# Performance work log

Measured on AMD Instinct MI355X. Metric: run time of the kernel, lower is better.

## Reference

```python
import jax, jax.numpy as jnp
import numpy as np

G = 8
NEIGHBORS = 9
EPS = 1e-5


def grid_sample_bilinear_border(img, grid):
    # img: [B, C, H, W], grid: [B, Hg, Wg, 2] with (x, y) in [-1, 1]
    # matches torch.nn.functional.grid_sample(mode='bilinear', padding_mode='border', align_corners=False)
    B, C, H, W = img.shape
    gx, gy = grid[..., 0], grid[..., 1]
    ix = jnp.clip(((gx + 1.0) * W - 1.0) * 0.5, 0.0, W - 1.0)
    iy = jnp.clip(((gy + 1.0) * H - 1.0) * 0.5, 0.0, H - 1.0)
    x0 = jnp.floor(ix); y0 = jnp.floor(iy)
    x1 = x0 + 1.0;      y1 = y0 + 1.0
    w00 = (x1 - ix) * (y1 - iy)
    w01 = (ix - x0) * (y1 - iy)
    w10 = (x1 - ix) * (iy - y0)
    w11 = (ix - x0) * (iy - y0)
    x0i = jnp.clip(x0, 0, W - 1).astype(jnp.int32)
    x1i = jnp.clip(x1, 0, W - 1).astype(jnp.int32)
    y0i = jnp.clip(y0, 0, H - 1).astype(jnp.int32)
    y1i = jnp.clip(y1, 0, H - 1).astype(jnp.int32)

    def gather(im, yy, xx):  # im [C,H,W], yy/xx [Hg,Wg] -> [C,Hg,Wg]
        return im[:, yy, xx]

    g = jax.vmap(gather)
    out = (g(img, y0i, x0i) * w00[:, None]
         + g(img, y0i, x1i) * w01[:, None]
         + g(img, y1i, x0i) * w10[:, None]
         + g(img, y1i, x1i) * w11[:, None])
    return out  # [B, C, Hg, Wg]


def pconv(x, w):
    # 1x1x1 conv3d (no bias): x [B,Cin,D,H,W], w [Cout,Cin]
    return jnp.einsum('bcdhw,oc->bodhw', x, w)


def bn_relu(x, gamma, beta):
    # BatchNorm3d (training-mode batch stats, biased variance) + ReLU
    mean = jnp.mean(x, axis=(0, 2, 3, 4), keepdims=True)
    var = jnp.var(x, axis=(0, 2, 3, 4), keepdims=True)
    xn = (x - mean) * jax.lax.rsqrt(var + EPS)
    return jax.nn.relu(xn * gamma.reshape(1, -1, 1, 1, 1) + beta.reshape(1, -1, 1, 1, 1))


def setup_inputs() -> dict:
    key = jax.random.key(0)
    ks = jax.random.split(key, 8)
    B, C, H, W = 2, 64, 256, 320
    ref_feature = jax.random.normal(ks[0], (B, C, H, W), dtype=jnp.float32)
    grid = jax.random.uniform(ks[1], (B, NEIGHBORS * H, W, 2), dtype=jnp.float32,
                              minval=-1.0, maxval=1.0)
    s0 = 1.0 / np.sqrt(G)
    w0 = jax.random.uniform(ks[2], (16, G), jnp.float32, -s0, s0)
    g0 = jnp.ones((16,), jnp.float32); b0 = jnp.zeros((16,), jnp.float32)
    s1 = 1.0 / np.sqrt(16)
    w1 = jax.random.uniform(ks[3], (8, 16), jnp.float32, -s1, s1)
    g1 = jnp.ones((8,), jnp.float32); b1 = jnp.zeros((8,), jnp.float32)
    s2 = 1.0 / np.sqrt(8)
    ws = jax.random.uniform(ks[4], (1, 8), jnp.float32, -s2, s2)
    bs = jax.random.uniform(ks[5], (1,), jnp.float32, -s2, s2)
    return {"ref_feature": ref_feature, "grid": grid,
            "w0": w0, "g0": g0, "b0": b0,
            "w1": w1, "g1": g1, "b1": b1,
            "ws": ws, "bs": bs}


def reference(ref_feature, grid, w0, g0, b0, w1, g1, b1, ws, bs):
    B, C, H, W = ref_feature.shape
    x = grid_sample_bilinear_border(ref_feature, grid)          # [B, C, 9H, W]
    ref = ref_feature.reshape(B, G, C // G, H, W)               # [B, G, C/G, H, W]
    x = x.reshape(B, G, C // G, NEIGHBORS, H, W)
    x = jnp.mean(x * ref[:, :, :, None], axis=2)                # [B, G, 9, H, W]
    x = bn_relu(pconv(x, w0), g0, b0)                           # [B, 16, 9, H, W]
    x = bn_relu(pconv(x, w1), g1, b1)                           # [B, 8, 9, H, W]
    s = pconv(x, ws) + bs.reshape(1, -1, 1, 1, 1)               # [B, 1, 9, H, W]
    return jax.nn.sigmoid(jnp.squeeze(s, axis=1))               # [B, 9, H, W]
```

## Files before the change

kernel.cpp:

```cpp
#include <hip/hip_runtime.h>
#include <math.h>


constexpr int   Bc  = 2;
constexpr int   Cc  = 64;
constexpr int   Hc  = 256;
constexpr int   Wc  = 320;
constexpr int   NBc = 9;
constexpr int   HWc = Hc * Wc;
constexpr int   NPIX = Bc * HWc;
constexpr int   NPT  = Bc * NBc * HWc;
constexpr float EPSV = 1e-5f;

constexpr int NB1 = 512;
constexpr int NB2 = 512;

constexpr size_t OFF_FEATB = 0;
constexpr size_t OFF_S     = OFF_FEATB + (size_t)NPIX * 32;
constexpr size_t OFF_P1    = OFF_S + (size_t)NPT * 8;
constexpr size_t OFF_BN1   = OFF_P1 + (size_t)NB1 * 32;
constexpr size_t OFF_P2    = OFF_BN1 + 32;
constexpr size_t OFF_BN2   = OFF_P2 + (size_t)NB2 * 16;

__device__ __forceinline__ unsigned short f2bf_rne(float v) {
  unsigned int u = __float_as_uint(v);
  unsigned int r = (u + 0x7fffu + ((u >> 16) & 1u)) >> 16;
  return (unsigned short)r;
}

__global__ __launch_bounds__(256) void k_transpose(
    const float* __restrict__ feat, unsigned short* __restrict__ featB) {
  __shared__ float lds[64][65];
  const int tid  = threadIdx.x;
  const int b    = blockIdx.x / (HWc / 64);
  const int tile = blockIdx.x % (HWc / 64);
  const int hw0  = tile * 64;
  const int p    = tid & 63;
  const int ty   = tid >> 6;

  const float* src = feat + (size_t)b * Cc * HWc + hw0 + p;
#pragma unroll
  for (int c0 = 0; c0 < 64; c0 += 4) {
    lds[c0 + ty][p] = src[(size_t)(c0 + ty) * HWc];
  }
  __syncthreads();
  const int ch = tid & 63;
  unsigned short* dst = featB + ((size_t)b * HWc + hw0) * 64 + ch;
#pragma unroll
  for (int p0 = 0; p0 < 64; p0 += 4) {
    dst[(size_t)(p0 + ty) * 64] = f2bf_rne(lds[ch][p0 + ty]);
  }
}

__device__ __forceinline__ void unpack8(uint4 u, float f[8]) {
  f[0] = __uint_as_float(u.x << 16);
  f[1] = __uint_as_float(u.x & 0xffff0000u);
  f[2] = __uint_as_float(u.y << 16);
  f[3] = __uint_as_float(u.y & 0xffff0000u);
  f[4] = __uint_as_float(u.z << 16);
  f[5] = __uint_as_float(u.z & 0xffff0000u);
  f[6] = __uint_as_float(u.w << 16);
  f[7] = __uint_as_float(u.w & 0xffff0000u);
}

__global__ __launch_bounds__(256) void k_sample(
    const float* __restrict__ grid, const unsigned short* __restrict__ featB,
    const float* __restrict__ feat, float* __restrict__ sOut) {
  const int tid = threadIdx.x;
  const int cid = blockIdx.x * 32 + (tid >> 3);
  const int j   = tid & 7;
  const int b   = cid / HWc;
  const int hw  = cid - b * HWc;
  const int h   = hw / Wc;
  const int w   = hw - h * Wc;

  const float* rp = feat + ((size_t)b * Cc + j * 8) * HWc + hw;
  float r[8];
#pragma unroll
  for (int k = 0; k < 8; ++k) r[k] = rp[(size_t)k * HWc];

  const uint4* fb = (const uint4*)featB + (size_t)b * HWc * 8;

#pragma unroll 3
  for (int n = 0; n < NBc; ++n) {
    const size_t gi = ((((size_t)b * NBc + n) * Hc + h) * Wc + w) * 2;
    const float2 g2 = *(const float2*)(grid + gi);
    float ix = ((g2.x + 1.f) * (float)Wc - 1.f) * 0.5f;
    float iy = ((g2.y + 1.f) * (float)Hc - 1.f) * 0.5f;
    ix = fminf(fmaxf(ix, 0.f), (float)(Wc - 1));
    iy = fminf(fmaxf(iy, 0.f), (float)(Hc - 1));
    const float x0f = floorf(ix), y0f = floorf(iy);
    const float fx = ix - x0f, fy = iy - y0f;
    const int x0 = (int)x0f, y0 = (int)y0f;
    const int x1 = min(x0 + 1, Wc - 1), y1 = min(y0 + 1, Hc - 1);
    const float w00 = (1.f - fx) * (1.f - fy);
    const float w01 = fx * (1.f - fy);
    const float w10 = (1.f - fx) * fy;
    const float w11 = fx * fy;

    const uint4 u00 = fb[(size_t)(y0 * Wc + x0) * 8 + j];
    const uint4 u01 = fb[(size_t)(y0 * Wc + x1) * 8 + j];
    const uint4 u10 = fb[(size_t)(y1 * Wc + x0) * 8 + j];
    const uint4 u11 = fb[(size_t)(y1 * Wc + x1) * 8 + j];
    float a[8], c[8], d[8], e[8];
    unpack8(u00, a);
    unpack8(u01, c);
    unpack8(u10, d);
    unpack8(u11, e);

    float s = 0.f;
#pragma unroll
    for (int k = 0; k < 8; ++k) {
      s += (w00 * a[k] + w01 * c[k] + w10 * d[k] + w11 * e[k]) * r[k];
    }
    s *= 0.125f;

    const size_t pt = ((size_t)b * NBc + n) * HWc + hw;
    sOut[pt * 8 + j] = s;
  }
}

__global__ __launch_bounds__(256) void k_stats1(
    const float* __restrict__ sBuf, const float* __restrict__ w0,
    float* __restrict__ partials) {
  __shared__ float w0s[128];
  __shared__ float red[4 * 32];
  const int tid = threadIdx.x;
  if (tid < 128) w0s[tid] = w0[tid];
  __syncthreads();

  float sy[16], sy2[16];
#pragma unroll
  for (int c = 0; c < 16; ++c) { sy[c] = 0.f; sy2[c] = 0.f; }

  const int stride = gridDim.x * blockDim.x;
  for (int p = blockIdx.x * blockDim.x + tid; p < NPT; p += stride) {
    const float4* sp = (const float4*)(sBuf + (size_t)p * 8);
    const float4 s0 = sp[0], s1 = sp[1];
#pragma unroll
    for (int c = 0; c < 16; ++c) {
      const float* wr = w0s + c * 8;
      const float y = wr[0] * s0.x + wr[1] * s0.y + wr[2] * s0.z + wr[3] * s0.w +
                      wr[4] * s1.x + wr[5] * s1.y + wr[6] * s1.z + wr[7] * s1.w;
      sy[c] += y;
      sy2[c] += y * y;
    }
  }
#pragma unroll
  for (int c = 0; c < 16; ++c) {
    for (int off = 32; off >= 1; off >>= 1) {
      sy[c] += __shfl_xor(sy[c], off);
      sy2[c] += __shfl_xor(sy2[c], off);
    }
  }
  const int wid = tid >> 6;
  if ((tid & 63) == 0) {
#pragma unroll
    for (int c = 0; c < 16; ++c) {
      red[wid * 32 + c] = sy[c];
      red[wid * 32 + 16 + c] = sy2[c];
    }
  }
  __syncthreads();
  if (tid < 32) {
    partials[(size_t)blockIdx.x * 32 + tid] =
        red[tid] + red[32 + tid] + red[64 + tid] + red[96 + tid];
  }
}

__global__ __launch_bounds__(256) void k_fin1(
    const float* __restrict__ partials, const float* __restrict__ g0,
    const float* __restrict__ b0, float* __restrict__ bn1) {
  __shared__ float acc[256];
  __shared__ float tot[32];
  const int tid = threadIdx.x;
  const int v = tid & 31, chunk = tid >> 5;
  float sm = 0.f;
  for (int b = chunk; b < NB1; b += 8) sm += partials[(size_t)b * 32 + v];
  acc[tid] = sm;
  __syncthreads();
  if (tid < 32) {
    float t = 0.f;
#pragma unroll
    for (int k = 0; k < 8; ++k) t += acc[k * 32 + tid];
    tot[tid] = t;
  }
  __syncthreads();
  if (tid < 16) {
    const float invN = 1.f / (float)NPT;
    const float mean = tot[tid] * invN;
    const float var = tot[tid + 16] * invN - mean * mean;
    const float a = g0[tid] * rsqrtf(var + EPSV);
    bn1[tid] = a;
    bn1[16 + tid] = b0[tid] - mean * a;
  }
}

__global__ __launch_bounds__(256) void k_stats2(
    const float* __restrict__ sBuf, const float* __restrict__ w0,
    const float* __restrict__ w1, const float* __restrict__ bn1,
    float* __restrict__ partials) {
  __shared__ float w0s[128], w1s[128], a1s[16], c1s[16];
  __shared__ float red[4 * 16];
  const int tid = threadIdx.x;
  if (tid < 128) { w0s[tid] = w0[tid]; w1s[tid] = w1[tid]; }
  if (tid < 16) { a1s[tid] = bn1[tid]; c1s[tid] = bn1[16 + tid]; }
  __syncthreads();

  float sz[8], sz2[8];
#pragma unroll
  for (int o = 0; o < 8; ++o) { sz[o] = 0.f; sz2[o] = 0.f; }

  const int stride = gridDim.x * blockDim.x;
  for (int p = blockIdx.x * blockDim.x + tid; p < NPT; p += stride) {
    const float4* sp = (const float4*)(sBuf + (size_t)p * 8);
    const float4 s0 = sp[0], s1 = sp[1];
    float x1[16];
#pragma unroll
    for (int c = 0; c < 16; ++c) {
      const float* wr = w0s + c * 8;
      const float y = wr[0] * s0.x + wr[1] * s0.y + wr[2] * s0.z + wr[3] * s0.w +
                      wr[4] * s1.x + wr[5] * s1.y + wr[6] * s1.z + wr[7] * s1.w;
      x1[c] = fmaxf(a1s[c] * y + c1s[c], 0.f);
    }
#pragma unroll
    for (int o = 0; o < 8; ++o) {
      const float* wr = w1s + o * 16;
      float z = 0.f;
#pragma unroll
      for (int k = 0; k < 16; ++k) z += wr[k] * x1[k];
      sz[o] += z;
      sz2[o] += z * z;
    }
  }
#pragma unroll
  for (int o = 0; o < 8; ++o) {
    for (int off = 32; off >= 1; off >>= 1) {
      sz[o] += __shfl_xor(sz[o], off);
      sz2[o] += __shfl_xor(sz2[o], off);
    }
  }
  const int wid = tid >> 6;
  if ((tid & 63) == 0) {
#pragma unroll
    for (int o = 0; o < 8; ++o) {
      red[wid * 16 + o] = sz[o];
      red[wid * 16 + 8 + o] = sz2[o];
    }
  }
  __syncthreads();
  if (tid < 16) {
    partials[(size_t)blockIdx.x * 16 + tid] =
        red[tid] + red[16 + tid] + red[32 + tid] + red[48 + tid];
  }
}

__global__ __launch_bounds__(256) void k_fin2(
    const float* __restrict__ partials, const float* __restrict__ g1,
    const float* __restrict__ b1, float* __restrict__ bn2) {
  __shared__ float acc[256];
  __shared__ float tot[16];
  const int tid = threadIdx.x;
  const int v = tid & 15, chunk = tid >> 4;
  float sm = 0.f;
  for (int b = chunk; b < NB2; b += 16) sm += partials[(size_t)b * 16 + v];
  acc[tid] = sm;
  __syncthreads();
  if (tid < 16) {
    float t = 0.f;
#pragma unroll
    for (int k = 0; k < 16; ++k) t += acc[k * 16 + tid];
    tot[tid] = t;
  }
  __syncthreads();
  if (tid < 8) {
    const float invN = 1.f / (float)NPT;
    const float mean = tot[tid] * invN;
    const float var = tot[tid + 8] * invN - mean * mean;
    const float a = g1[tid] * rsqrtf(var + EPSV);
    bn2[tid] = a;
    bn2[8 + tid] = b1[tid] - mean * a;
  }
}

__global__ __launch_bounds__(256) void k_final(
    const float* __restrict__ sBuf, const float* __restrict__ w0,
    const float* __restrict__ w1, const float* __restrict__ bn1,
    const float* __restrict__ bn2, const float* __restrict__ wsW,
    const float* __restrict__ bs, float* __restrict__ out) {
  __shared__ float w0s[128], w1s[128], a1s[16], c1s[16], a2s[8], c2s[8], wss[8];
  __shared__ float bss;
  const int tid = threadIdx.x;
  if (tid < 128) { w0s[tid] = w0[tid]; w1s[tid] = w1[tid]; }
  if (tid < 16) { a1s[tid] = bn1[tid]; c1s[tid] = bn1[16 + tid]; }
  if (tid < 8) { a2s[tid] = bn2[tid]; c2s[tid] = bn2[8 + tid]; wss[tid] = wsW[tid]; }
  if (tid == 0) bss = bs[0];
  __syncthreads();

  const int p = blockIdx.x * blockDim.x + tid;
  if (p >= NPT) return;
  const float4* sp = (const float4*)(sBuf + (size_t)p * 8);
  const float4 s0 = sp[0], s1 = sp[1];
  float x1[16];
#pragma unroll
  for (int c = 0; c < 16; ++c) {
    const float* wr = w0s + c * 8;
    const float y = wr[0] * s0.x + wr[1] * s0.y + wr[2] * s0.z + wr[3] * s0.w +
                    wr[4] * s1.x + wr[5] * s1.y + wr[6] * s1.z + wr[7] * s1.w;
    x1[c] = fmaxf(a1s[c] * y + c1s[c], 0.f);
  }
  float o = bss;
#pragma unroll
  for (int oc = 0; oc < 8; ++oc) {
    const float* wr = w1s + oc * 16;
    float z = 0.f;
#pragma unroll
    for (int k = 0; k < 16; ++k) z += wr[k] * x1[k];
    const float x2 = fmaxf(a2s[oc] * z + c2s[oc], 0.f);
    o += wss[oc] * x2;
  }
  out[p] = 1.f / (1.f + expf(-o));
}

extern "C" void kernel_launch(void* const* d_in, const int* in_sizes, int n_in,
                              void* d_out, int out_size, void* d_ws,
                              size_t ws_size, hipStream_t stream) {
  const float* feat = (const float*)d_in[0];
  const float* grid = (const float*)d_in[1];
  const float* w0 = (const float*)d_in[2];
  const float* g0 = (const float*)d_in[3];
  const float* b0 = (const float*)d_in[4];
  const float* w1 = (const float*)d_in[5];
  const float* g1 = (const float*)d_in[6];
  const float* b1 = (const float*)d_in[7];
  const float* wsW = (const float*)d_in[8];
  const float* bs = (const float*)d_in[9];
  float* out = (float*)d_out;

  float* wsf = (float*)d_ws;
  unsigned short* featB = (unsigned short*)(wsf + OFF_FEATB);
  float* sBuf  = wsf + OFF_S;
  float* p1    = wsf + OFF_P1;
  float* bn1   = wsf + OFF_BN1;
  float* p2    = wsf + OFF_P2;
  float* bn2   = wsf + OFF_BN2;

  k_transpose<<<Bc * (HWc / 64), 256, 0, stream>>>(feat, featB);
  k_sample<<<NPIX / 32, 256, 0, stream>>>(grid, featB, feat, sBuf);
  k_stats1<<<NB1, 256, 0, stream>>>(sBuf, w0, p1);
  k_fin1<<<1, 256, 0, stream>>>(p1, g0, b0, bn1);
  k_stats2<<<NB2, 256, 0, stream>>>(sBuf, w0, w1, bn1, p2);
  k_fin2<<<1, 256, 0, stream>>>(p2, g1, b1, bn2);
  k_final<<<NPT / 256, 256, 0, stream>>>(sBuf, w0, w1, bn1, bn2, wsW, bs, out);
}
```

Measured before the change: 283.2 us.

## Fuse first BN statistics into sampling kernel and parallelize finalizers

The layer-1 BatchNorm sum and sum-of-squares are now computed inside the sampling kernel from an LDS copy of each block's sampled values, so the separate stats1 pass no longer re-reads the whole sample buffer. Per-block partials are stored channel-major and reduced by one block per channel with wave shuffles instead of a single block. The reference features now come from the bf16 transposed copy rather than the strided fp32 tensor. This adds LDS use, an occupancy hint and a barrier to the sampler, and the reference values lose precision by being rounded to bf16.

```diff
diff --git a/kernel.cpp b/kernel.cpp
--- a/kernel.cpp
+++ b/kernel.cpp
@@ -12,20 +12,31 @@
 constexpr int   NPT  = Bc * NBc * HWc;
 constexpr float EPSV = 1e-5f;
 
-constexpr int NB1 = 512;
-constexpr int NB2 = 512;
+constexpr int NBLK_S = NPIX / 32;
+constexpr int NB2    = 512;
 
 constexpr size_t OFF_FEATB = 0;
 constexpr size_t OFF_S     = OFF_FEATB + (size_t)NPIX * 32;
-constexpr size_t OFF_P1    = OFF_S + (size_t)NPT * 8;
-constexpr size_t OFF_BN1   = OFF_P1 + (size_t)NB1 * 32;
-constexpr size_t OFF_P2    = OFF_BN1 + 32;
-constexpr size_t OFF_BN2   = OFF_P2 + (size_t)NB2 * 16;
+constexpr size_t OFF_PT    = OFF_S + (size_t)NPT * 8;
+constexpr size_t OFF_BN1   = OFF_PT + (size_t)32 * NBLK_S;
+constexpr size_t OFF_P2T   = OFF_BN1 + 32;
+constexpr size_t OFF_BN2   = OFF_P2T + (size_t)16 * NB2;
 
 __device__ __forceinline__ unsigned short f2bf_rne(float v) {
   unsigned int u = __float_as_uint(v);
   unsigned int r = (u + 0x7fffu + ((u >> 16) & 1u)) >> 16;
   return (unsigned short)r;
+}
+
+__device__ __forceinline__ void unpack8(uint4 u, float f[8]) {
+  f[0] = __uint_as_float(u.x << 16);
+  f[1] = __uint_as_float(u.x & 0xffff0000u);
+  f[2] = __uint_as_float(u.y << 16);
+  f[3] = __uint_as_float(u.y & 0xffff0000u);
+  f[4] = __uint_as_float(u.z << 16);
+  f[5] = __uint_as_float(u.z & 0xffff0000u);
+  f[6] = __uint_as_float(u.w << 16);
+  f[7] = __uint_as_float(u.w & 0xffff0000u);
 }
 
 __global__ __launch_bounds__(256) void k_transpose(
@@ -52,34 +63,30 @@
   }
 }
 
-__device__ __forceinline__ void unpack8(uint4 u, float f[8]) {
-  f[0] = __uint_as_float(u.x << 16);
-  f[1] = __uint_as_float(u.x & 0xffff0000u);
-  f[2] = __uint_as_float(u.y << 16);
-  f[3] = __uint_as_float(u.y & 0xffff0000u);
-  f[4] = __uint_as_float(u.z << 16);
-  f[5] = __uint_as_float(u.z & 0xffff0000u);
-  f[6] = __uint_as_float(u.w << 16);
-  f[7] = __uint_as_float(u.w & 0xffff0000u);
-}
-
-__global__ __launch_bounds__(256) void k_sample(
+__global__ __launch_bounds__(256, 6) void k_sample(
     const float* __restrict__ grid, const unsigned short* __restrict__ featB,
-    const float* __restrict__ feat, float* __restrict__ sOut) {
-  const int tid = threadIdx.x;
-  const int cid = blockIdx.x * 32 + (tid >> 3);
+    const float* __restrict__ w0, float* __restrict__ sOut,
+    float* __restrict__ pT) {
+  __shared__ float sL[288 * 9];
+  __shared__ float w0s[128];
+  __shared__ float red[4 * 32];
+  const int tid = threadIdx.x;
+  const int pix = tid >> 3;
+  const int cid = blockIdx.x * 32 + pix;
   const int j   = tid & 7;
   const int b   = cid / HWc;
   const int hw  = cid - b * HWc;
   const int h   = hw / Wc;
   const int w   = hw - h * Wc;
 
-  const float* rp = feat + ((size_t)b * Cc + j * 8) * HWc + hw;
+  if (tid < 128) w0s[tid] = w0[tid];
+
+  const uint4* fbAll = (const uint4*)featB;
+  const uint4 ur = fbAll[(size_t)cid * 8 + j];
   float r[8];
-#pragma unroll
-  for (int k = 0; k < 8; ++k) r[k] = rp[(size_t)k * HWc];
-
-  const uint4* fb = (const uint4*)featB + (size_t)b * HWc * 8;
+  unpack8(ur, r);
+
+  const uint4* fb = fbAll + (size_t)b * HWc * 8;
 
 #pragma unroll 3
   for (int n = 0; n < NBc; ++n) {
@@ -117,31 +124,22 @@
 
     const size_t pt = ((size_t)b * NBc + n) * HWc + hw;
     sOut[pt * 8 + j] = s;
-  }
-}
-
-__global__ __launch_bounds__(256) void k_stats1(
-    const float* __restrict__ sBuf, const float* __restrict__ w0,
-    float* __restrict__ partials) {
-  __shared__ float w0s[128];
-  __shared__ float red[4 * 32];
-  const int tid = threadIdx.x;
-  if (tid < 128) w0s[tid] = w0[tid];
+    sL[(n * 32 + pix) * 9 + j] = s;
+  }
   __syncthreads();
 
   float sy[16], sy2[16];
 #pragma unroll
   for (int c = 0; c < 16; ++c) { sy[c] = 0.f; sy2[c] = 0.f; }
-
-  const int stride = gridDim.x * blockDim.x;
-  for (int p = blockIdx.x * blockDim.x + tid; p < NPT; p += stride) {
-    const float4* sp = (const float4*)(sBuf + (size_t)p * 8);
-    const float4 s0 = sp[0], s1 = sp[1];
+  for (int p = tid; p < 288; p += 256) {
+    float sv[8];
+#pragma unroll
+    for (int k = 0; k < 8; ++k) sv[k] = sL[p * 9 + k];
 #pragma unroll
     for (int c = 0; c < 16; ++c) {
       const float* wr = w0s + c * 8;
-      const float y = wr[0] * s0.x + wr[1] * s0.y + wr[2] * s0.z + wr[3] * s0.w +
-                      wr[4] * s1.x + wr[5] * s1.y + wr[6] * s1.z + wr[7] * s1.w;
+      float y = wr[0] * sv[0] + wr[1] * sv[1] + wr[2] * sv[2] + wr[3] * sv[3] +
+                wr[4] * sv[4] + wr[5] * sv[5] + wr[6] * sv[6] + wr[7] * sv[7];
       sy[c] += y;
       sy2[c] += y * y;
     }
@@ -163,43 +161,44 @@
   }
   __syncthreads();
   if (tid < 32) {
-    partials[(size_t)blockIdx.x * 32 + tid] =
+    pT[(size_t)tid * NBLK_S + blockIdx.x] =
         red[tid] + red[32 + tid] + red[64 + tid] + red[96 + tid];
   }
 }
 
 __global__ __launch_bounds__(256) void k_fin1(
-    const float* __restrict__ partials, const float* __restrict__ g0,
+    const float* __restrict__ pT, const float* __restrict__ g0,
     const float* __restrict__ b0, float* __restrict__ bn1) {
-  __shared__ float acc[256];
-  __shared__ float tot[32];
-  const int tid = threadIdx.x;
-  const int v = tid & 31, chunk = tid >> 5;
-  float sm = 0.f;
-  for (int b = chunk; b < NB1; b += 8) sm += partials[(size_t)b * 32 + v];
-  acc[tid] = sm;
-  __syncthreads();
-  if (tid < 32) {
-    float t = 0.f;
-#pragma unroll
-    for (int k = 0; k < 8; ++k) t += acc[k * 32 + tid];
-    tot[tid] = t;
-  }
-  __syncthreads();
-  if (tid < 16) {
+  __shared__ float red[8];
+  const int tid = threadIdx.x;
+  const int c = blockIdx.x;
+  float sa = 0.f, sb = 0.f;
+  for (int i = tid; i < NBLK_S; i += 256) {
+    sa += pT[(size_t)c * NBLK_S + i];
+    sb += pT[(size_t)(16 + c) * NBLK_S + i];
+  }
+  for (int off = 32; off >= 1; off >>= 1) {
+    sa += __shfl_xor(sa, off);
+    sb += __shfl_xor(sb, off);
+  }
+  if ((tid & 63) == 0) { red[(tid >> 6) * 2] = sa; red[(tid >> 6) * 2 + 1] = sb; }
+  __syncthreads();
+  if (tid == 0) {
+    const float ta = red[0] + red[2] + red[4] + red[6];
+    const float tb = red[1] + red[3] + red[5] + red[7];
     const float invN = 1.f / (float)NPT;
-    const float mean = tot[tid] * invN;
-    const float var = tot[tid + 16] * invN - mean * mean;
-    const float a = g0[tid] * rsqrtf(var + EPSV);
-    bn1[tid] = a;
-    bn1[16 + tid] = b0[tid] - mean * a;
+    const float mean = ta * invN;
+    const float var = tb * invN - mean * mean;
+    const float a = g0[c] * rsqrtf(var + EPSV);
+    bn1[c] = a;
+    bn1[16 + c] = b0[c] - mean * a;
   }
 }
 
 __global__ __launch_bounds__(256) void k_stats2(
     const float* __restrict__ sBuf, const float* __restrict__ w0,
     const float* __restrict__ w1, const float* __restrict__ bn1,
-    float* __restrict__ partials) {
+    float* __restrict__ p2T) {
   __shared__ float w0s[128], w1s[128], a1s[16], c1s[16];
   __shared__ float red[4 * 16];
   const int tid = threadIdx.x;
@@ -250,36 +249,37 @@
   }
   __syncthreads();
   if (tid < 16) {
-    partials[(size_t)blockIdx.x * 16 + tid] =
+    p2T[(size_t)tid * NB2 + blockIdx.x] =
         red[tid] + red[16 + tid] + red[32 + tid] + red[48 + tid];
   }
 }
 
 __global__ __launch_bounds__(256) void k_fin2(
-    const float* __restrict__ partials, const float* __restrict__ g1,
+    const float* __restrict__ p2T, const float* __restrict__ g1,
     const float* __restrict__ b1, float* __restrict__ bn2) {
-  __shared__ float acc[256];
-  __shared__ float tot[16];
-  const int tid = threadIdx.x;
-  const int v = tid & 15, chunk = tid >> 4;
-  float sm = 0.f;
-  for (int b = chunk; b < NB2; b += 16) sm += partials[(size_t)b * 16 + v];
-  acc[tid] = sm;
-  __syncthreads();
-  if (tid < 16) {
-    float t = 0.f;
-#pragma unroll
-    for (int k = 0; k < 16; ++k) t += acc[k * 16 + tid];
-    tot[tid] = t;
-  }
-  __syncthreads();
-  if (tid < 8) {
+  __shared__ float red[8];
+  const int tid = threadIdx.x;
+  const int c = blockIdx.x;
+  float sa = 0.f, sb = 0.f;
+  for (int i = tid; i < NB2; i += 256) {
+    sa += p2T[(size_t)c * NB2 + i];
+    sb += p2T[(size_t)(8 + c) * NB2 + i];
+  }
+  for (int off = 32; off >= 1; off >>= 1) {
+    sa += __shfl_xor(sa, off);
+    sb += __shfl_xor(sb, off);
+  }
+  if ((tid & 63) == 0) { red[(tid >> 6) * 2] = sa; red[(tid >> 6) * 2 + 1] = sb; }
+  __syncthreads();
+  if (tid == 0) {
+    const float ta = red[0] + red[2] + red[4] + red[6];
+    const float tb = red[1] + red[3] + red[5] + red[7];
     const float invN = 1.f / (float)NPT;
-    const float mean = tot[tid] * invN;
-    const float var = tot[tid + 8] * invN - mean * mean;
-    const float a = g1[tid] * rsqrtf(var + EPSV);
-    bn2[tid] = a;
-    bn2[8 + tid] = b1[tid] - mean * a;
+    const float mean = ta * invN;
+    const float var = tb * invN - mean * mean;
+    const float a = g1[c] * rsqrtf(var + EPSV);
+    bn2[c] = a;
+    bn2[8 + c] = b1[c] - mean * a;
   }
 }
 
@@ -339,17 +339,16 @@
 
   float* wsf = (float*)d_ws;
   unsigned short* featB = (unsigned short*)(wsf + OFF_FEATB);
-  float* sBuf  = wsf + OFF_S;
-  float* p1    = wsf + OFF_P1;
-  float* bn1   = wsf + OFF_BN1;
-  float* p2    = wsf + OFF_P2;
-  float* bn2   = wsf + OFF_BN2;
+  float* sBuf = wsf + OFF_S;
+  float* pT   = wsf + OFF_PT;
+  float* bn1  = wsf + OFF_BN1;
+  float* p2T  = wsf + OFF_P2T;
+  float* bn2  = wsf + OFF_BN2;
 
   k_transpose<<<Bc * (HWc / 64), 256, 0, stream>>>(feat, featB);
-  k_sample<<<NPIX / 32, 256, 0, stream>>>(grid, featB, feat, sBuf);
-  k_stats1<<<NB1, 256, 0, stream>>>(sBuf, w0, p1);
-  k_fin1<<<1, 256, 0, stream>>>(p1, g0, b0, bn1);
-  k_stats2<<<NB2, 256, 0, stream>>>(sBuf, w0, w1, bn1, p2);
-  k_fin2<<<1, 256, 0, stream>>>(p2, g1, b1, bn2);
-  k_final<<<NPT / 256, 256, 0, stream>>>(sBuf, w0, w1, bn1, bn2, wsW, bs, out);
-}
+  k_sample<<<NBLK_S, 256, 0, stream>>>(grid, featB, w0, sBuf, pT);
+  k_fin1<<<16, 256, 0, stream>>>(pT, g0, b0, bn1);
+  k_stats2<<<NB2, 256, 0, stream>>>(sBuf, w0, w1, bn1, p2T);
+  k_fin2<<<8, 256, 0, stream>>>(p2T, g1, b1, bn2);
+  k_final<<<(NPT + 255) / 256, 256, 0, stream>>>(sBuf, w0, w1, bn1, bn2, wsW, bs, out);
+}
```

After: 485.4 us. 71.4% more time.
